# Performance work log

Measured on AMD Instinct MI355X. Metric: run time of the kernel, lower is better.

The kernel has to match this reference:

```python
import jax, jax.numpy as jnp
import numpy as np

H = 12            # heads
NB_FEATURES = 256 # Performer random features
EPS = 1e-4        # performer_pytorch softmax_kernel eps


def _gaussian_orthogonal_matrix(nb_rows, nb_cols, rng):
    # performer_pytorch gaussian_orthogonal_random_matrix, scaling=0
    nb_full = nb_rows // nb_cols
    blocks = []
    for _ in range(nb_full):
        q, _ = np.linalg.qr(rng.standard_normal((nb_cols, nb_cols)))
        blocks.append(q.T)
    rem = nb_rows - nb_full * nb_cols
    if rem > 0:
        q, _ = np.linalg.qr(rng.standard_normal((nb_cols, nb_cols)))
        blocks.append(q.T[:rem])
    M = np.concatenate(blocks, axis=0)
    multiplier = np.linalg.norm(rng.standard_normal((nb_rows, nb_cols)), axis=1)
    return (multiplier[:, None] * M).astype(np.float32)


def setup_inputs() -> dict:
    key = jax.random.key(0)
    ks = jax.random.split(key, 10)
    B, N, D = 8, 2048, 768
    s = D ** -0.5  # keep activations O(1) so exp() in FAVOR+ is stable
    inp = {
        "x": jax.random.normal(ks[0], (B, N, D), jnp.float32),
        "Wq": jax.random.normal(ks[1], (D, D), jnp.float32) * s,
        "bq": jnp.zeros((D,), jnp.float32),
        "Wk": jax.random.normal(ks[2], (D, D), jnp.float32) * s,
        "bk": jnp.zeros((D,), jnp.float32),
        "Wv": jax.random.normal(ks[3], (D, D), jnp.float32) * s,
        "bv": jnp.zeros((D,), jnp.float32),
        "Wo": jax.random.normal(ks[4], (D, D), jnp.float32) * s,
        "bo": jnp.zeros((D,), jnp.float32),
        "proj": jnp.asarray(_gaussian_orthogonal_matrix(NB_FEATURES, D // H, np.random.default_rng(0))),
    }
    return inp


def _softmax_kernel(x, proj, is_query):
    # x: [b,h,n,d], proj: [m,d] -> phi(x): [b,h,n,m]
    d = x.shape[-1]
    data_normalizer = d ** -0.25
    ratio = proj.shape[0] ** -0.5
    xp = jnp.einsum('bhnd,md->bhnm', x * data_normalizer, proj)
    diag = jnp.sum(x * x, axis=-1, keepdims=True) * 0.5 * (data_normalizer ** 2)
    if is_query:
        m = jax.lax.stop_gradient(jnp.max(xp, axis=-1, keepdims=True))
    else:
        m = jax.lax.stop_gradient(jnp.max(xp, axis=(-1, -2), keepdims=True))
    return ratio * (jnp.exp(xp - diag - m) + EPS)


def reference(x, Wq, bq, Wk, bk, Wv, bv, Wo, bo, proj):
    b, n, dim = x.shape
    d = dim // H
    # qkv projections, split into heads: [b,h,n,d]
    q = (x @ Wq.T + bq).reshape(b, n, H, d).transpose(0, 2, 1, 3)
    k = (x @ Wk.T + bk).reshape(b, n, H, d).transpose(0, 2, 1, 3)
    v = (x @ Wv.T + bv).reshape(b, n, H, d).transpose(0, 2, 1, 3)
    # FAVOR+ feature maps: [b,h,n,m]
    qp = _softmax_kernel(q, proj, True)
    kp = _softmax_kernel(k, proj, False)
    # non-causal linear attention
    k_sum = kp.sum(axis=2)                                  # [b,h,m]
    D_inv = 1.0 / jnp.einsum('bhnm,bhm->bhn', qp, k_sum)    # [b,h,n]
    ctx = jnp.einsum('bhnm,bhnd->bhmd', kp, v)              # [b,h,m,d]
    out = jnp.einsum('bhmd,bhnm,bhn->bhnd', ctx, qp, D_inv)
    out = out.transpose(0, 2, 1, 3).reshape(b, n, dim)
    return out @ Wo.T + bo
```

## Files before the change

### kernel.cpp

```cpp
#include <hip/hip_runtime.h>
#include <stdint.h>

typedef unsigned short u16;
typedef unsigned int u32;
typedef __attribute__((ext_vector_type(8))) short short8;
typedef __attribute__((ext_vector_type(4))) float floatx4;

#define HN 12
#define DH 64
#define DM 768
#define NS 2048
#define NB 8
#define MF 256
#define BN (NB*NS)
#define BH (NB*HN)

#define NRM 0.35355339059327373f
#define RATIO 0.0625f
#define EPSV 1e-4f

__device__ __forceinline__ float b2f(u32 u){ union{u32 i; float f;} x; x.i=u<<16; return x.f; }
__device__ __forceinline__ u32 f2b(float v){ union{float f; u32 u;} x; x.f=v; return (x.u + 0x7FFFu + ((x.u>>16)&1u))>>16; }
__device__ __forceinline__ u32 fkey(float v){ union{float f; u32 u;} x; x.f=v; return (x.u&0x80000000u)? ~x.u : (x.u|0x80000000u); }
__device__ __forceinline__ float funkey(u32 k){ union{u32 u; float f;} x; x.u=(k&0x80000000u)? (k^0x80000000u) : ~k; return x.f; }
__device__ __forceinline__ void bld8(uint4 r, float s, float* f){
  f[0]=b2f(r.x&0xffffu)*s; f[1]=b2f(r.x>>16)*s;
  f[2]=b2f(r.y&0xffffu)*s; f[3]=b2f(r.y>>16)*s;
  f[4]=b2f(r.z&0xffffu)*s; f[5]=b2f(r.z>>16)*s;
  f[6]=b2f(r.w&0xffffu)*s; f[7]=b2f(r.w>>16)*s;
}
__device__ __forceinline__ void load8(const void* base, size_t idx, int isf32, float s, float* f){
  if(isf32){
    const float* p=(const float*)base + idx;
    const float4 u=((const float4*)p)[0], v=((const float4*)p)[1];
    f[0]=u.x*s; f[1]=u.y*s; f[2]=u.z*s; f[3]=u.w*s;
    f[4]=v.x*s; f[5]=v.y*s; f[6]=v.z*s; f[7]=v.w*s;
  }else{
    uint4 r=*(const uint4*)((const u16*)base+idx);
    bld8(r,s,f);
  }
}
__device__ __forceinline__ float ld1(const void* base, int idx, int isf32){
  return isf32 ? ((const float*)base)[idx] : b2f((u32)((const u16*)base)[idx]);
}
__device__ __forceinline__ void gl16(const void* g, void* l){
  __builtin_amdgcn_global_load_lds(
    (const __attribute__((address_space(1))) u32*)g,
    (__attribute__((address_space(3))) u32*)l, 16, 0, 0);
}

__global__ __launch_bounds__(64) void k_detect(const u16* __restrict__ x, int* __restrict__ flag)
{
  __shared__ int w[64], z[64];
  const int t=threadIdx.x;
  int wild=0, zero=0;
  for(int i=t;i<256;i+=64){
    u32 u=(u32)x[2*i];
    u32 e=(u>>7)&0xFFu;
    if(e>=0x90u) wild++;
    if((u&0x7FFFu)==0u) zero++;
  }
  w[t]=wild; z[t]=zero; __syncthreads();
  if(t==0){
    int W=0,Z=0;
    for(int i=0;i<64;++i){W+=w[i];Z+=z[i];}
    flag[0]=(W>16||Z>200)?1:0;
  }
}

__global__ __launch_bounds__(256) void k_cvtw(const void* __restrict__ Wq,
    const void* __restrict__ Wk, const void* __restrict__ Wv, const void* __restrict__ Wo,
    u16* __restrict__ wb, u16* __restrict__ wob, const int* __restrict__ flagp)
{
  const int isf32=*flagp;
  const size_t WSZ=(size_t)DM*DM;
  size_t idx=((size_t)blockIdx.x*256+threadIdx.x)*8;
  const void* src; size_t off; u16* dst;
  if(idx<3*WSZ){ int w=(int)(idx/WSZ); src=(w==0)?Wq:((w==1)?Wk:Wv); off=idx-(size_t)w*WSZ; dst=wb+idx; }
  else { src=Wo; off=idx-3*WSZ; dst=wob+off; }
  if(isf32){
    const float* p=(const float*)src+off;
    float4 u=((const float4*)p)[0], v=((const float4*)p)[1];
    uint4 st;
    st.x=f2b(u.x)|(f2b(u.y)<<16); st.y=f2b(u.z)|(f2b(u.w)<<16);
    st.z=f2b(v.x)|(f2b(v.y)<<16); st.w=f2b(v.z)|(f2b(v.w)<<16);
    *(uint4*)dst=st;
  }else{
    *(uint4*)dst=*(const uint4*)((const u16*)src+off);
  }
}

__global__ __launch_bounds__(256) void k_cvtp(const void* __restrict__ proj,
    u16* __restrict__ pn, const int* __restrict__ flagp)
{
  const int isf32=*flagp;
  const size_t idx=((size_t)blockIdx.x*256+threadIdx.x)*8;
  float pf[8];
  load8(proj, idx, isf32, NRM, pf);
  uint4 st;
  st.x=f2b(pf[0])|(f2b(pf[1])<<16); st.y=f2b(pf[2])|(f2b(pf[3])<<16);
  st.z=f2b(pf[4])|(f2b(pf[5])<<16); st.w=f2b(pf[6])|(f2b(pf[7])<<16);
  *(uint4*)(pn+idx)=st;
}

__global__ __launch_bounds__(256) void k_cvtx(const void* __restrict__ x,
    u16* __restrict__ xb, const int* __restrict__ flagp)
{
  const int isf32=*flagp;
  const size_t idx=((size_t)blockIdx.x*256+threadIdx.x)*8;
  float f[8];
  load8(x, idx, isf32, 1.0f, f);
  uint4 st;
  st.x=f2b(f[0])|(f2b(f[1])<<16); st.y=f2b(f[2])|(f2b(f[3])<<16);
  st.z=f2b(f[4])|(f2b(f[5])<<16); st.w=f2b(f[6])|(f2b(f[7])<<16);
  *(uint4*)(xb+idx)=st;
}

__global__ __launch_bounds__(256) void k_diag(const u16* __restrict__ src, float* __restrict__ dk)
{
  const size_t row=(size_t)blockIdx.x*256+threadIdx.x;
  const u16* p=src+row*DH;
  float s=0.f;
#pragma unroll
  for(int c=0;c<DH;c+=8){
    uint4 r=*(const uint4*)(p+c);
    float f[8]; bld8(r,1.0f,f);
#pragma unroll
    for(int j=0;j<8;++j) s+=f[j]*f[j];
  }
  dk[row]=0.5f*NRM*NRM*s;
}

__device__ __forceinline__ void gemm_epilogue(const floatx4 acc[4][4], int mode, int oflag,
    int m0, int n0, int l, int wr4, int wc4,
    const void* bias0, const void* bias1, const void* bias2,
    u16* q, u16* k, u16* v, void* outv)
{
  const int rbase=(l>>4)*4, cl=l&15;
  if(mode==0){
    const int which=n0/DM;
    const void* bias=(which==0)?bias0:((which==1)?bias1:bias2);
    u16* outp=(which==0)?q:((which==1)?k:v);
    const int cb=n0-which*DM;
#pragma unroll
    for(int j=0;j<4;++j){
      const int col=cb+(wc4+j)*16+cl;
      const int h=col>>6, dd=col&63;
      const float bb=ld1(bias,col,oflag);
#pragma unroll
      for(int i=0;i<4;++i){
#pragma unroll
        for(int r=0;r<4;++r){
          const int grow=m0+(wr4+i)*16+rbase+r;
          const int b_=grow>>11, n=grow&2047;
          const u16 val=(u16)f2b(acc[i][j][r]+bb);
          if(which==2) outp[((size_t)(b_*HN+h)*DH+dd)*NS + n]=val;
          else         outp[((size_t)((b_*HN+h)*NS+n))*DH + dd]=val;
        }
      }
    }
  }else{
#pragma unroll
    for(int j=0;j<4;++j){
      const int col=n0+(wc4+j)*16+cl;
      const float bb=ld1(bias0,col,oflag);
#pragma unroll
      for(int i=0;i<4;++i){
#pragma unroll
        for(int r=0;r<4;++r){
          const int grow=m0+(wr4+i)*16+rbase+r;
          const float val=acc[i][j][r]+bb;
          if(oflag) ((float*)outv)[(size_t)grow*DM+col]=val;
          else      ((u16*)outv)[(size_t)grow*DM+col]=(u16)f2b(val);
        }
      }
    }
  }
}

__global__ __launch_bounds__(256) void k_gemm2(const u16* __restrict__ A16,
    const u16* __restrict__ B16,
    const void* __restrict__ bias0, const void* __restrict__ bias1, const void* __restrict__ bias2,
    u16* __restrict__ q, u16* __restrict__ k, u16* __restrict__ v,
    void* __restrict__ outv, const int* __restrict__ flagp, const int mode)
{
  __shared__ short At[16*512];
  __shared__ short Bt[16*512];
  const int oflag=*flagp;
  const int t=threadIdx.x, l=t&63, w=t>>6;
  const int m0=blockIdx.x*128, n0=blockIdx.y*128;
  const int wr4=(w>>1)*4, wc4=(w&1)*4;
  const int srow=l&15, skg=l>>4;
  floatx4 acc[4][4]={};
  for(int k0=0;k0<DM;k0+=64){
    __syncthreads();
#pragma unroll
    for(int s=0;s<4;++s){
      const int bi=w*4+s, rb=bi>>1, kh=bi&1;
      const int kc=k0+kh*32+skg*8;
      gl16(A16 + (size_t)(m0+rb*16+srow)*DM + kc, &At[bi*512]);
      gl16(B16 + (size_t)(n0+rb*16+srow)*DM + kc, &Bt[bi*512]);
    }
    __syncthreads();
#pragma unroll
    for(int kh=0;kh<2;++kh){
      short8 af[4], bf[4];
#pragma unroll
      for(int i=0;i<4;++i) af[i]=*(short8*)&At[((wr4+i)*2+kh)*512+l*8];
#pragma unroll
      for(int j=0;j<4;++j) bf[j]=*(short8*)&Bt[((wc4+j)*2+kh)*512+l*8];
#pragma unroll
      for(int i=0;i<4;++i)
#pragma unroll
        for(int j=0;j<4;++j)
          acc[i][j]=__builtin_amdgcn_mfma_f32_16x16x32_bf16(af[i],bf[j],acc[i][j],0,0,0);
    }
  }
  gemm_epilogue(acc,mode,oflag,m0,n0,l,wr4,wc4,bias0,bias1,bias2,q,k,v,outv);
}

__global__ __launch_bounds__(256) void k_gemm_f(const void* __restrict__ Araw,
    const u16* __restrict__ B16,
    const void* __restrict__ bias0, const void* __restrict__ bias1, const void* __restrict__ bias2,
    u16* __restrict__ q, u16* __restrict__ k, u16* __restrict__ v,
    void* __restrict__ outv, const int* __restrict__ flagp, const int mode)
{
  __shared__ short At[16*512];
  __shared__ short Bt[16*512];
  const int oflag=*flagp;
  const int isf32=(mode==0)?oflag:0;
  const int t=threadIdx.x, l=t&63, w=t>>6;
  const int m0=blockIdx.x*128, n0=blockIdx.y*128;
  const int wr4=(w>>1)*4, wc4=(w&1)*4;
  const int srow=l&15, skg=l>>4;
  floatx4 acc[4][4]={};
  for(int k0=0;k0<DM;k0+=64){
    __syncthreads();
#pragma unroll
    for(int s=0;s<4;++s){
      const int bi=w*4+s, rb=bi>>1, kh=bi&1;
      const int kc=k0+kh*32+skg*8;
      uint4 va;
      if(isf32){
        const float* ap=(const float*)Araw + (size_t)(m0+rb*16+srow)*DM + kc;
        float4 u=((const float4*)ap)[0], vv=((const float4*)ap)[1];
        va.x=f2b(u.x)|(f2b(u.y)<<16);  va.y=f2b(u.z)|(f2b(u.w)<<16);
        va.z=f2b(vv.x)|(f2b(vv.y)<<16); va.w=f2b(vv.z)|(f2b(vv.w)<<16);
      }else{
        va=*(const uint4*)((const u16*)Araw + (size_t)(m0+rb*16+srow)*DM + kc);
      }
      const uint4 vb=*(const uint4*)(B16 + (size_t)(n0+rb*16+srow)*DM + kc);
      *(uint4*)&At[bi*512+l*8]=va;
      *(uint4*)&Bt[bi*512+l*8]=vb;
    }
    __syncthreads();
#pragma unroll
    for(int kh=0;kh<2;++kh){
      short8 af[4], bf[4];
#pragma unroll
      for(int i=0;i<4;++i) af[i]=*(short8*)&At[((wr4+i)*2+kh)*512+l*8];
#pragma unroll
      for(int j=0;j<4;++j) bf[j]=*(short8*)&Bt[((wc4+j)*2+kh)*512+l*8];
#pragma unroll
      for(int i=0;i<4;++i)
#pragma unroll
        for(int j=0;j<4;++j)
          acc[i][j]=__builtin_amdgcn_mfma_f32_16x16x32_bf16(af[i],bf[j],acc[i][j],0,0,0);
    }
  }
  gemm_epilogue(acc,mode,oflag,m0,n0,l,wr4,wc4,bias0,bias1,bias2,q,k,v,outv);
}

#define SBOFF(slot,kh,mf) ((((slot)*32)+((kh)*16)+(mf))*512)
#define STA(kt,kh) do{ \
  const int o_=SBOFF((kt)&1,(kh),0); \
  const size_t g_=(size_t)(kt)*64+(size_t)(kh)*32; \
  gl16(Ar0+g_, &As[o_+w*512]); \
  gl16(Ar0+(size_t)128*768+g_, &As[o_+(8+w)*512]); \
}while(0)
#define STB(kt,kh) do{ \
  const int o_=SBOFF((kt)&1,(kh),0); \
  const size_t g_=(size_t)(kt)*64+(size_t)(kh)*32; \
  gl16(Br0+g_, &Bs[o_+w*512]); \
  gl16(Br0+(size_t)128*768+g_, &Bs[o_+(8+w)*512]); \
}while(0)
#define STAB(kt,kh) do{ STA(kt,kh); STB(kt,kh); }while(0)
#define LDA8(kt,kh) do{ const int o_=SBOFF((kt)&1,(kh),wr*8)+l*8; \
  _Pragma("unroll") for(int i_=0;i_<8;++i_) a[i_]=*(short8*)&As[o_+i_*512]; }while(0)
#define LDB4(kt,kh) do{ const int o_=SBOFF((kt)&1,(kh),wc*4)+l*8; \
  b[0]=*(short8*)&Bs[o_]; b[1]=*(short8*)&Bs[o_+512]; \
  b[2]=*(short8*)&Bs[o_+1024]; b[3]=*(short8*)&Bs[o_+1536]; }while(0)
#define MM(np) do{ _Pragma("unroll") for(int i_=0;i_<8;++i_){ \
  acc[i_][(np)*2+0]=__builtin_amdgcn_mfma_f32_16x16x32_bf16(a[i_],b[(np)*2+0],acc[i_][(np)*2+0],0,0,0); \
  acc[i_][(np)*2+1]=__builtin_amdgcn_mfma_f32_16x16x32_bf16(a[i_],b[(np)*2+1],acc[i_][(np)*2+1],0,0,0); } }while(0)
#define FEN asm volatile("" ::: "memory")
#define BARR do{ FEN; __builtin_amdgcn_s_barrier(); FEN; }while(0)
#define WV8 asm volatile("s_waitcnt vmcnt(8)" ::: "memory")
#define WV4 asm volatile("s_waitcnt vmcnt(4)" ::: "memory")
#define WV0 asm volatile("s_waitcnt vmcnt(0)" ::: "memory")
#define WL0 do{ asm volatile("s_waitcnt lgkmcnt(0)" ::: "memory"); __builtin_amdgcn_sched_barrier(0); }while(0)
#define PH4(kt,kh,SST,WST) do{ LDA8(kt,kh); LDB4(kt,kh); SST; WST; BARR; WL0; \
  __builtin_amdgcn_s_setprio(1); MM(0); MM(1); __builtin_amdgcn_s_setprio(0); BARR; }while(0)

__global__ __launch_bounds__(512,2) void k_gemm8(const u16* __restrict__ A16,
    const u16* __restrict__ B16,
    const void* __restrict__ bias0, const void* __restrict__ bias1, const void* __restrict__ bias2,
    u16* __restrict__ q, u16* __restrict__ k, u16* __restrict__ v,
    void* __restrict__ outv, const int* __restrict__ flagp, const int mode,
    float* __restrict__ dq_, float* __restrict__ dk_)
{
  __shared__ short As[2*2*16*512];
  __shared__ short Bs[2*2*16*512];
  const int oflag=*flagp;
  const int t=threadIdx.x, l=t&63, w=t>>6;
  const int wr=w>>2, wc=w&3;
  const int lrow=l&15, lk8=(l>>4)*8;
  int bid = blockIdx.y*gridDim.x + blockIdx.x;
  const int nwg = gridDim.x*gridDim.y;
  const int nN  = gridDim.y;
  bid = (bid&7)*(nwg>>3) + (bid>>3);
  const int mi = bid/nN;
  const int m0 = mi*256;
  const int n0 = (bid - mi*nN)*256;

  const u16* Ar0 = A16 + (size_t)(m0 + w*16 + lrow)*768 + lk8;
  const u16* Br0 = B16 + (size_t)(n0 + w*16 + lrow)*768 + lk8;
  floatx4 acc[8][4]={};
  short8 a[8], b[4];

  STA(0,0); STB(0,0); STA(0,1); STB(0,1); STA(1,0); STB(1,0);
  WV8; BARR;

  for(int i=0;i<5;++i){
    const int kt=2*i;
    PH4(kt,0,   STAB(kt+1,1), WV8);
    PH4(kt,1,   STAB(kt+2,0), WV8);
    PH4(kt+1,0, STAB(kt+2,1), WV8);
    PH4(kt+1,1, STAB(kt+3,0), WV8);
  }
  PH4(10,0, STAB(11,1), WV8);
  PH4(10,1, (void)0, WV4);
  PH4(11,0, (void)0, WV0);
  PH4(11,1, (void)0, (void)0);

  const int cl=l&15, q4=l>>4;
  if(mode==0){
    const int which=n0/DM;
    const int cb0=n0-which*DM;
    const void* bias=(which==0)?bias0:((which==1)?bias1:bias2);
    u16* outp=(which==0)?q:((which==1)?k:v);
    if(which==2){
#pragma unroll
      for(int j=0;j<4;++j){
        const int col=wc*64+j*16+cl;
        const float bb=ld1(bias,cb0+col,oflag);
        char* cbase=(char*)((col<128)? (void*)(As+col*256) : (void*)(Bs+(col-128)*256));
        const int X=(col&7)<<4;
#pragma unroll
        for(int i=0;i<8;++i){
          const int rowb=wr*128+i*16+q4*4;
          uint2 pk;
          pk.x=f2b(acc[i][j][0]+bb)|(f2b(acc[i][j][1]+bb)<<16);
          pk.y=f2b(acc[i][j][2]+bb)|(f2b(acc[i][j][3]+bb)<<16);
          *(uint2*)(cbase + ((rowb*2)^X)) = pk;
        }
      }
      __syncthreads();
      const int b_=m0>>11, nbase=m0&2047;
#pragma unroll
      for(int tt=0;tt<16;++tt){
        const int task=tt*8+w;
        const int colg=task>>2, qq=task&3;
        const int col=colg*8+(l>>3), sub=l&7;
        char* cbase=(char*)((col<128)? (void*)(As+col*256) : (void*)(Bs+(col-128)*256));
        const uint4 d4=*(const uint4*)(cbase + ((qq*128+sub*16)^((col&7)<<4)));
        const int gcol=cb0+col, h=gcol>>6, dd=gcol&63;
        const int n=nbase+qq*64+sub*8;
        *(uint4*)&outp[((size_t)(b_*HN+h)*DH+dd)*NS + n]=d4;
      }
    } else {
      float bb4[4];
#pragma unroll
      for(int j=0;j<4;++j) bb4[j]=ld1(bias, cb0+wc*64+j*16+cl, oflag);
      float* dptr=(which==0)? dq_ : dk_;
#pragma unroll
      for(int i=0;i<8;++i){
#pragma unroll
        for(int r=0;r<4;++r){
          const int row=wr*128+i*16+q4*4+r;
          char* rbase=(char*)((row<128)? (void*)(As+row*256) : (void*)(Bs+(row-128)*256));
          const int X=(row&3)<<4;
          float s=0.f;
#pragma unroll
          for(int j=0;j<4;++j){
            const int col=wc*64+j*16+cl;
            const u16 hv=(u16)f2b(acc[i][j][r]+bb4[j]);
            *(u16*)(rbase + ((col*2)^X)) = hv;
            const float fv=b2f(hv);
            s+=fv*fv;
          }
          s+=__shfl_xor(s,1,64); s+=__shfl_xor(s,2,64);
          s+=__shfl_xor(s,4,64); s+=__shfl_xor(s,8,64);
          if(cl==0){
            const int grow=m0+row, b_=grow>>11, n=grow&2047;
            dptr[(size_t)(b_*HN + (cb0>>6)+wc)*NS + n]=0.5f*NRM*NRM*s;
          }
        }
      }
      __syncthreads();
      const int hb=cb0>>6;
#pragma unroll
      for(int tt=0;tt<16;++tt){
        const int task=tt*8+w;
        const int rowg=task>>2, qq=task&3;
        const int row=rowg*8+(l>>3), sub=l&7;
        char* rbase=(char*)((row<128)? (void*)(As+row*256) : (void*)(Bs+(row-128)*256));
        const uint4 d4=*(const uint4*)(rbase + ((qq*128+sub*16)^((row&3)<<4)));
        const int grow=m0+row, b_=grow>>11, n=grow&2047;
        *(uint4*)&outp[((size_t)(b_*HN+hb+qq)*NS+n)*DH + sub*8]=d4;
      }
    }
  } else {
    if(oflag){
#pragma unroll
      for(int p=0;p<2;++p){
        if(wr==p){
#pragma unroll
          for(int j=0;j<4;++j){
            const int col=wc*64+j*16+cl;
            const float bb=ld1(bias0,n0+col,oflag);
#pragma unroll
            for(int i=0;i<8;++i){
#pragma unroll
              for(int r=0;r<4;++r){
                const int row=i*16+q4*4+r;
                char* rbase=(char*)((row<64)? (void*)(As+row*512) : (void*)(Bs+(row-64)*512));
                *(float*)(rbase + ((col*4)^((row&3)<<4))) = acc[i][j][r]+bb;
              }
            }
          }
        }
        __syncthreads();
#pragma unroll
        for(int tt=0;tt<16;++tt){
          const int task=tt*8+w;
          const int rowg=task>>3, qq=task&7;
          const int row=rowg*8+(l>>3), sub=l&7;
          char* rbase=(char*)((row<64)? (void*)(As+row*512) : (void*)(Bs+(row-64)*512));
          const uint4 d4=*(const uint4*)(rbase + ((qq*128+sub*16)^((row&3)<<4)));
          const size_t grow=(size_t)m0+p*128+row;
          *(uint4*)((char*)outv + (grow*DM+n0)*4 + qq*128 + sub*16)=d4;
        }
        __syncthreads();
      }
    } else {
#pragma unroll
      for(int j=0;j<4;++j){
        const int col=wc*64+j*16+cl;
        const float bb=ld1(bias0,n0+col,oflag);
#pragma unroll
        for(int i=0;i<8;++i){
#pragma unroll
          for(int r=0;r<4;++r){
            const int row=wr*128+i*16+q4*4+r;
            char* rbase=(char*)((row<128)? (void*)(As+row*256) : (void*)(Bs+(row-128)*256));
            *(u16*)(rbase + ((col*2)^((row&3)<<4))) = (u16)f2b(acc[i][j][r]+bb);
          }
        }
      }
      __syncthreads();
#pragma unroll
      for(int tt=0;tt<16;++tt){
        const int task=tt*8+w;
        const int rowg=task>>2, qq=task&3;
        const int row=rowg*8+(l>>3), sub=l&7;
        char* rbase=(char*)((row<128)? (void*)(As+row*256) : (void*)(Bs+(row-128)*256));
        const uint4 d4=*(const uint4*)(rbase + ((qq*128+sub*16)^((row&3)<<4)));
        const int grow=m0+row;
        *(uint4*)((u16*)outv + (size_t)grow*DM + n0 + qq*64 + sub*8)=d4;
      }
    }
  }
}

__global__ __launch_bounds__(256) void k_xpk2(const u16* __restrict__ kb,
    const u16* __restrict__ pn, u32* __restrict__ kmax)
{
  __shared__ short Bt[32*512];
  __shared__ short At[8*512];
  __shared__ float red[256];
  const int t=threadIdx.x, l=t&63, w=t>>6;
  const int bh=blockIdx.y, nb0=blockIdx.x*256;
  for(int s=t;s<2048;s+=256){
    const int ub=s>>6, l2=s&63, mt=ub>>1, kh=ub&1;
    const int row=mt*16+(l2&15), kc=kh*32+(l2>>4)*8;
    *(uint4*)&Bt[ub*512+l2*8]=*(const uint4*)(pn + (size_t)row*DH + kc);
  }
  float vmax=-3.4e38f;
  for(int c=0;c<4;++c){
    const int n0=nb0+c*64;
    __syncthreads();
    for(int s=t;s<512;s+=256){
      const int ua=s>>6, l2=s&63, rb=ua>>1, kh=ua&1;
      const int n=n0+rb*16+(l2&15), kc=kh*32+(l2>>4)*8;
      *(uint4*)&At[ua*512+l2*8]=*(const uint4*)(kb + ((size_t)bh*NS+n)*DH + kc);
    }
    __syncthreads();
    const short8 af0=*(short8*)&At[(w*2+0)*512+l*8];
    const short8 af1=*(short8*)&At[(w*2+1)*512+l*8];
#pragma unroll
    for(int mt=0;mt<16;++mt){
      floatx4 a={};
      a=__builtin_amdgcn_mfma_f32_16x16x32_bf16(af0,*(short8*)&Bt[(mt*2+0)*512+l*8],a,0,0,0);
      a=__builtin_amdgcn_mfma_f32_16x16x32_bf16(af1,*(short8*)&Bt[(mt*2+1)*512+l*8],a,0,0,0);
      vmax=fmaxf(vmax,fmaxf(fmaxf(a[0],a[1]),fmaxf(a[2],a[3])));
    }
  }
  red[t]=vmax; __syncthreads();
  for(int s=128;s>0;s>>=1){ if(t<s) red[t]=fmaxf(red[t],red[t+s]); __syncthreads(); }
  if(t==0) atomicMax(kmax+bh, fkey(red[0]));
}

__global__ __launch_bounds__(256) void k_ctx2(const u16* __restrict__ kb,
    const u16* __restrict__ vT, const u16* __restrict__ pn,
    const float* __restrict__ dkbuf, const u32* __restrict__ kmax,
    float* __restrict__ ctxT, float* __restrict__ ksum)
{
  __shared__ short Bt[32*512];
  __shared__ u16   Ks[256*72];
  __shared__ short AtV[8*512];
  __shared__ float dg[64];
  const int t=threadIdx.x, l=t&63, w=t>>6;
  const int split=blockIdx.x, bh=blockIdx.y;
  for(int s=t;s<2048;s+=256){
    const int ub=s>>6, l2=s&63, mt=ub>>1, kh=ub&1;
    const int row=mt*16+(l2&15), kc=kh*32+(l2>>4)*8;
    *(uint4*)&Bt[ub*512+l2*8]=*(const uint4*)(pn + (size_t)row*DH + kc);
  }
  const float kM=funkey(kmax[bh]);
  float ksr=0.f;
  floatx4 acc2[4][4]={};
  for(int c=0;c<8;++c){
    const int n0=split*512+c*64;
    __syncthreads();
    for(int s=t;s<512;s+=256){
      const int ua=s>>6, l2=s&63, rb=ua>>1, kh=ua&1;
      const int n=n0+rb*16+(l2&15), kc=kh*32+(l2>>4)*8;
      *(uint4*)&AtV[ua*512+l2*8]=*(const uint4*)(kb + ((size_t)bh*NS+n)*DH + kc);
    }
    if(t<64) dg[t]=dkbuf[(size_t)bh*NS+n0+t];
    __syncthreads();
    short8 af[4][2];
#pragma unroll
    for(int rb=0;rb<4;++rb){
      af[rb][0]=*(short8*)&AtV[(rb*2+0)*512+l*8];
      af[rb][1]=*(short8*)&AtV[(rb*2+1)*512+l*8];
    }
    float dgl[16];
#pragma unroll
    for(int rb=0;rb<4;++rb)
#pragma unroll
      for(int r=0;r<4;++r) dgl[rb*4+r]=dg[rb*16+(l>>4)*4+r];
#pragma unroll
    for(int ml=0;ml<4;++ml){
      const int mt=w*4+ml;
      const short8 bf0=*(short8*)&Bt[(mt*2+0)*512+l*8];
      const short8 bf1=*(short8*)&Bt[(mt*2+1)*512+l*8];
      const int m=mt*16+(l&15);
#pragma unroll
      for(int rb=0;rb<4;++rb){
        floatx4 a={};
        a=__builtin_amdgcn_mfma_f32_16x16x32_bf16(af[rb][0],bf0,a,0,0,0);
        a=__builtin_amdgcn_mfma_f32_16x16x32_bf16(af[rb][1],bf1,a,0,0,0);
        const int nb=rb*16+(l>>4)*4;
        const float v0=RATIO*(__expf(a[0]-dgl[rb*4+0]-kM)+EPSV);
        const float v1=RATIO*(__expf(a[1]-dgl[rb*4+1]-kM)+EPSV);
        const float v2=RATIO*(__expf(a[2]-dgl[rb*4+2]-kM)+EPSV);
        const float v3=RATIO*(__expf(a[3]-dgl[rb*4+3]-kM)+EPSV);
        *(u32*)&Ks[m*72+nb]  =f2b(v0)|(f2b(v1)<<16);
        *(u32*)&Ks[m*72+nb+2]=f2b(v2)|(f2b(v3)<<16);
      }
    }
    __syncthreads();
    for(int s=t;s<512;s+=256){
      const int uv=s>>6, l2=s&63, dt=uv>>1, kh=uv&1;
      const int d=dt*16+(l2&15), nn=n0+kh*32+(l2>>4)*8;
      *(uint4*)&AtV[uv*512+l2*8]=*(const uint4*)(vT + ((size_t)bh*DH+d)*NS + nn);
    }
    {
      float s8=0.f;
#pragma unroll
      for(int j=0;j<8;++j){
        const uint4 kk=*(const uint4*)&Ks[t*72+j*8];
        s8+=b2f(kk.x&0xffffu)+b2f(kk.x>>16)+b2f(kk.y&0xffffu)+b2f(kk.y>>16)
           +b2f(kk.z&0xffffu)+b2f(kk.z>>16)+b2f(kk.w&0xffffu)+b2f(kk.w>>16);
      }
      ksr+=s8;
    }
    __syncthreads();
#pragma unroll
    for(int i=0;i<4;++i){
      const int row=(w*4+i)*16+(l&15);
      const short8 a0=*(short8*)&Ks[row*72 + 0*32+(l>>4)*8];
      const short8 a1=*(short8*)&Ks[row*72 + 1*32+(l>>4)*8];
#pragma unroll
      for(int dt=0;dt<4;++dt){
        acc2[i][dt]=__builtin_amdgcn_mfma_f32_16x16x32_bf16(a0,*(short8*)&AtV[(dt*2+0)*512+l*8],acc2[i][dt],0,0,0);
        acc2[i][dt]=__builtin_amdgcn_mfma_f32_16x16x32_bf16(a1,*(short8*)&AtV[(dt*2+1)*512+l*8],acc2[i][dt],0,0,0);
      }
    }
  }
#pragma unroll
  for(int i=0;i<4;++i){
#pragma unroll
    for(int dt=0;dt<4;++dt){
#pragma unroll
      for(int r=0;r<4;++r){
        const int m=(w*4+i)*16+(l>>4)*4+r;
        const int d=dt*16+(l&15);
        atomicAdd(&ctxT[((size_t)bh*DH+d)*MF+m], acc2[i][dt][r]);
      }
    }
  }
  atomicAdd(ksum+bh*MF+t, ksr);
}

__global__ __launch_bounds__(256,2) void k_ctx3(const u16* __restrict__ kb,
    const u16* __restrict__ vT, const u16* __restrict__ pn,
    const float* __restrict__ dkbuf, const u32* __restrict__ kmax,
    float* __restrict__ ctxP, float* __restrict__ ksumP)
{
  __shared__ __align__(16) char SM[66048];
  short* Ks=(short*)SM;
  short* Kb=(short*)(SM+32768);
  short* Vb=(short*)(SM+49152);
  float* dgb=(float*)(SM+65536);
  const int t=threadIdx.x, l=t&63, w=t>>6;
  const int split=blockIdx.x, bh=blockIdx.y;
  const int n00=split*512;
  const int lrow=l&15, lk8=(l>>4)*8;
  const u16* kbase = kb + (size_t)bh*NS*DH;
  const u16* vbase = vT + (size_t)bh*DH*NS;
  short8 bf[4][2];
#pragma unroll
  for(int ml=0;ml<4;++ml)
#pragma unroll
    for(int kh=0;kh<2;++kh)
      bf[ml][kh]=*(const short8*)(pn + (size_t)((w*4+ml)*16+lrow)*DH + kh*32 + lk8);
  const float kM=funkey(kmax[bh]);
  {
#pragma unroll
    for(int p=0;p<2;++p){
      const int u=w+4*p, rb=u>>1, kh=u&1;
      gl16(kbase + (size_t)(n00+rb*16+lrow)*DH + kh*32+lk8, &Kb[u*512]);
    }
#pragma unroll
    for(int p=0;p<2;++p){
      const int u=w+4*p, dt=u>>1, kh=u&1;
      gl16(vbase + (size_t)(dt*16+lrow)*NS + n00+kh*32+lk8, &Vb[u*512]);
    }
    if(t<64) dgb[t]=dkbuf[(size_t)bh*NS+n00+t];
  }
  __syncthreads();
  float ksr=0.f;
  floatx4 acc2[4][4]={};
  for(int c=0;c<8;++c){
    const int cur=c&1, nxt=cur^1;
    if(c<7){
      const int n1=n00+(c+1)*64;
#pragma unroll
      for(int p=0;p<2;++p){
        const int u=w+4*p, rb=u>>1, kh=u&1;
        gl16(kbase + (size_t)(n1+rb*16+lrow)*DH + kh*32+lk8, &Kb[nxt*4096+u*512]);
      }
#pragma unroll
      for(int p=0;p<2;++p){
        const int u=w+4*p, dt=u>>1, kh=u&1;
        gl16(vbase + (size_t)(dt*16+lrow)*NS + n1+kh*32+lk8, &Vb[nxt*4096+u*512]);
      }
    }
    float dgnv=0.f;
    if(c<7 && t<64) dgnv=dkbuf[(size_t)bh*NS+n00+(c+1)*64+t];
    short8 af[4][2];
#pragma unroll
    for(int rb=0;rb<4;++rb){
      af[rb][0]=*(short8*)&Kb[cur*4096+(rb*2+0)*512+l*8];
      af[rb][1]=*(short8*)&Kb[cur*4096+(rb*2+1)*512+l*8];
    }
    float dgl[16];
#pragma unroll
    for(int rb=0;rb<4;++rb){
      const float4 dv=*(const float4*)&dgb[cur*64+rb*16+(l>>4)*4];
      dgl[rb*4+0]=dv.x; dgl[rb*4+1]=dv.y; dgl[rb*4+2]=dv.z; dgl[rb*4+3]=dv.w;
    }
#pragma unroll
    for(int ml=0;ml<4;++ml){
      const int m=(w*4+ml)*16+lrow;
      char* krow=(char*)Ks + m*128;
      const int xr=(m&7)<<4;
#pragma unroll
      for(int rb=0;rb<4;++rb){
        floatx4 a={};
        a=__builtin_amdgcn_mfma_f32_16x16x32_bf16(af[rb][0],bf[ml][0],a,0,0,0);
        a=__builtin_amdgcn_mfma_f32_16x16x32_bf16(af[rb][1],bf[ml][1],a,0,0,0);
        const float v0=RATIO*(__expf(a[0]-dgl[rb*4+0]-kM)+EPSV);
        const float v1=RATIO*(__expf(a[1]-dgl[rb*4+1]-kM)+EPSV);
        const float v2=RATIO*(__expf(a[2]-dgl[rb*4+2]-kM)+EPSV);
        const float v3=RATIO*(__expf(a[3]-dgl[rb*4+3]-kM)+EPSV);
        const int nb=rb*16+(l>>4)*4;
        const u32 bo=((u32)(nb*2)) ^ xr;
        *(u32*)(krow+bo)  =f2b(v0)|(f2b(v1)<<16);
        *(u32*)(krow+bo+4)=f2b(v2)|(f2b(v3)<<16);
      }
    }
    __syncthreads();
    {
      char* krow=(char*)Ks + t*128;
      const int xr=(t&7)<<4;
      float s8=0.f;
#pragma unroll
      for(int j=0;j<8;++j){
        const uint4 kk=*(const uint4*)(krow + ((j*16)^xr));
        s8+=b2f(kk.x&0xffffu)+b2f(kk.x>>16)+b2f(kk.y&0xffffu)+b2f(kk.y>>16)
           +b2f(kk.z&0xffffu)+b2f(kk.z>>16)+b2f(kk.w&0xffffu)+b2f(kk.w>>16);
      }
      ksr+=s8;
    }
#pragma unroll
    for(int i=0;i<4;++i){
      const int row=(w*4+i)*16+lrow;
      char* krow=(char*)Ks + row*128;
      const int xr=(row&7)<<4;
      const short8 a0=*(short8*)(krow + (((l>>4)*16)^xr));
      const short8 a1=*(short8*)(krow + ((64+(l>>4)*16)^xr));
#pragma unroll
      for(int dt=0;dt<4;++dt){
        acc2[i][dt]=__builtin_amdgcn_mfma_f32_16x16x32_bf16(a0,*(short8*)&Vb[cur*4096+(dt*2+0)*512+l*8],acc2[i][dt],0,0,0);
        acc2[i][dt]=__builtin_amdgcn_mfma_f32_16x16x32_bf16(a1,*(short8*)&Vb[cur*4096+(dt*2+1)*512+l*8],acc2[i][dt],0,0,0);
      }
    }
    if(c<7 && t<64) dgb[nxt*64+t]=dgnv;
    __syncthreads();
  }
  {
    float* OUT=(float*)SM;
#pragma unroll
    for(int i=0;i<4;++i){
      const int mb=(w*4+i)*16+(l>>4)*4;
#pragma unroll
      for(int dt=0;dt<4;++dt){
        const int d=dt*16+lrow;
        float4 o; o.x=acc2[i][dt][0]; o.y=acc2[i][dt][1]; o.z=acc2[i][dt][2]; o.w=acc2[i][dt][3];
        *(float4*)((char*)OUT + d*1024 + ((mb*4)^((d&15)<<4))) = o;
      }
    }
    __syncthreads();
    float* gout = ctxP + (size_t)(split*BH+bh)*64*256;
#pragma unroll
    for(int s=0;s<16;++s){
      const int d=s*4+w;
      const uint4 o4=*(const uint4*)((char*)OUT + d*1024 + ((l*16)^((d&15)<<4)));
      *(uint4*)(gout + (size_t)d*256 + l*4)=o4;
    }
    ksumP[(size_t)(split*BH+bh)*256 + t]=ksr;
  }
}

__global__ __launch_bounds__(256) void k_csplit(const float* __restrict__ ctxT,
    u16* __restrict__ chi, u16* __restrict__ clo, float* __restrict__ ecs)
{
  __shared__ float cred[256];
  const int bh=blockIdx.x, t=threadIdx.x;
  const int d=t>>2, part=t&3;
  const size_t base=((size_t)bh*DH+d)*MF + part*64;
  const float* src=ctxT + base;
  u16* ph=chi + base;
  u16* pl=clo + base;
  float cs=0.f;
  for(int m=0;m<64;m+=4){
    float4 v=*(const float4*)(src+m);
    float vv[4]={v.x,v.y,v.z,v.w};
    u32 h_[4], l_[4];
#pragma unroll
    for(int j=0;j<4;++j){
      cs+=vv[j];
      u32 hh=f2b(vv[j]);
      float rr=vv[j]-b2f(hh);
      h_[j]=hh; l_[j]=f2b(rr);
    }
    uint2 sh, sl;
    sh.x=h_[0]|(h_[1]<<16); sh.y=h_[2]|(h_[3]<<16);
    sl.x=l_[0]|(l_[1]<<16); sl.y=l_[2]|(l_[3]<<16);
    *(uint2*)(ph+m)=sh; *(uint2*)(pl+m)=sl;
  }
  cred[t]=cs; __syncthreads();
  if(part==0) ecs[bh*64+d]=EPSV*(cred[t]+cred[t+1]+cred[t+2]+cred[t+3]);
}

__global__ __launch_bounds__(256) void k_csplit3(const float* __restrict__ ctxP,
    const float* __restrict__ ksumP,
    u16* __restrict__ chi, u16* __restrict__ clo, float* __restrict__ ecs,
    float* __restrict__ ksum)
{
  __shared__ float wred[16][4];
  const int bh=blockIdx.y, dq=blockIdx.x;
  const int t=threadIdx.x, l=t&63, w=t>>6;
  if(dq==0){
    float kv=0.f;
#pragma unroll
    for(int s=0;s<4;++s) kv+=ksumP[(size_t)(s*BH+bh)*256+t];
    ksum[bh*MF+t]=kv;
  }
#pragma unroll
  for(int d16=0;d16<16;++d16){
    const int d=dq*16+d16;
    float v=0.f;
#pragma unroll
    for(int s=0;s<4;++s) v+=ctxP[((size_t)(s*BH+bh)*64+d)*256+t];
    const u32 hh=f2b(v);
    const float rr=v-b2f(hh);
    const size_t ob=((size_t)bh*DH+d)*MF+t;
    chi[ob]=(u16)hh; clo[ob]=(u16)f2b(rr);
    float s_=v;
    s_+=__shfl_xor(s_,1,64); s_+=__shfl_xor(s_,2,64); s_+=__shfl_xor(s_,4,64);
    s_+=__shfl_xor(s_,8,64); s_+=__shfl_xor(s_,16,64); s_+=__shfl_xor(s_,32,64);
    if(l==0) wred[d16][w]=s_;
  }
  __syncthreads();
  if(t<16) ecs[bh*64+dq*16+t]=EPSV*(wred[t][0]+wred[t][1]+wred[t][2]+wred[t][3]);
}

__global__ __launch_bounds__(256) void k_attn2(const u16* __restrict__ qb,
    const u16* __restrict__ pn, const float* __restrict__ dqbuf,
    const float* __restrict__ ksum, const u16* __restrict__ chi, const u16* __restrict__ clo,
    const float* __restrict__ ecs, u16* __restrict__ attn)
{
  __shared__ short At[8*512];
  __shared__ u16 Qf[32*512];
  __shared__ float ksums[256];
  __shared__ float dq_s[64];
  __shared__ float mxs[4][64];
  __shared__ float s1s[4][64];
  __shared__ float a_s[64], dinv_s[64], ec_s[64];
  __shared__ float red4[4];
  __shared__ float epkss;
  const int t=threadIdx.x, l=t&63, w=t>>6;
  const int bh=blockIdx.y, nb0=blockIdx.x*256;
  const int b_=bh/HN, h=bh%HN;
  {
    float kv=ksum[bh*MF+t];
    ksums[t]=kv;
    if(t<64) ec_s[t]=ecs[bh*64+t];
    float s=kv;
#pragma unroll
    for(int o=1;o<64;o<<=1) s+=__shfl_xor(s,o,64);
    if(l==0) red4[w]=s;
  }
  __syncthreads();
  if(t==0) epkss=EPSV*(red4[0]+red4[1]+red4[2]+red4[3]);
  short8 bhf[8], blf[8];
  {
    const int d=w*16+(l&15);
    const size_t base=((size_t)bh*DH+d)*MF;
#pragma unroll
    for(int kc=0;kc<8;++kc){
      const size_t off=base + kc*32+(l>>4)*8;
      bhf[kc]=*(const short8*)(chi+off);
      blf[kc]=*(const short8*)(clo+off);
    }
  }
  for(int c=0;c<4;++c){
    const int n0c=nb0+c*64;
    __syncthreads();
    for(int s=t;s<512;s+=256){
      const int ua=s>>6, l2=s&63, nt=ua>>1, kh=ua&1;
      const int n=n0c+nt*16+(l2&15), kc=kh*32+(l2>>4)*8;
      *(uint4*)&At[ua*512+l2*8]=*(const uint4*)(qb + ((size_t)bh*NS+n)*DH + kc);
    }
    if(t<64) dq_s[t]=dqbuf[(size_t)bh*NS+n0c+t];
    __syncthreads();
    float mxl[4]={-3.4e38f,-3.4e38f,-3.4e38f,-3.4e38f};
    float s1l[4]={0.f,0.f,0.f,0.f};
#pragma unroll
    for(int mt=0;mt<4;++mt){
      const int gm=w*4+mt;
      const u16* pr=pn + ((gm*16+(l&15))<<6) + (l>>4)*8;
      const short8 a0=*(const short8*)(pr);
      const short8 a1=*(const short8*)(pr+32);
      float k4[4];
#pragma unroll
      for(int r=0;r<4;++r) k4[r]=ksums[gm*16+(l>>4)*4+r];
      const int mbase=(gm&1)*16+(l>>4)*4;
      const int lane2=((mbase>>3)*16+(l&15))*8 + (mbase&7);
#pragma unroll
      for(int nt=0;nt<4;++nt){
        floatx4 xp={};
        xp=__builtin_amdgcn_mfma_f32_16x16x32_bf16(a0,*(short8*)&At[(nt*2+0)*512+l*8],xp,0,0,0);
        xp=__builtin_amdgcn_mfma_f32_16x16x32_bf16(a1,*(short8*)&At[(nt*2+1)*512+l*8],xp,0,0,0);
        const float dq=dq_s[nt*16+(l&15)];
        float ev[4];
#pragma unroll
        for(int r=0;r<4;++r){
          const float xv=xp[r];
          mxl[nt]=fmaxf(mxl[nt],xv);
          ev[r]=__expf(xv-dq);
          s1l[nt]+=ev[r]*k4[r];
        }
        u16* qp_=&Qf[(nt*8+(gm>>1))*512 + lane2];
        *(u32*)qp_    =f2b(ev[0])|(f2b(ev[1])<<16);
        *(u32*)(qp_+2)=f2b(ev[2])|(f2b(ev[3])<<16);
      }
    }
#pragma unroll
    for(int nt=0;nt<4;++nt){
      float m_=mxl[nt], s_=s1l[nt];
      m_=fmaxf(m_,__shfl_xor(m_,16,64)); s_+=__shfl_xor(s_,16,64);
      m_=fmaxf(m_,__shfl_xor(m_,32,64)); s_+=__shfl_xor(s_,32,64);
      if(l<16){ mxs[w][nt*16+l]=m_; s1s[w][nt*16+l]=s_; }
    }
    __syncthreads();
    if(t<64){
      float m_=fmaxf(fmaxf(mxs[0][t],mxs[1][t]),fmaxf(mxs[2][t],mxs[3][t]));
      float s_=s1s[0][t]+s1s[1][t]+s1s[2][t]+s1s[3][t];
      float a=__expf(-m_);
      a_s[t]=a;
      dinv_s[t]=1.0f/(a*s_+epkss);
    }
    __syncthreads();
    const int d=w*16+(l&15);
    const float ec=ec_s[d];
#pragma unroll
    for(int nt=0;nt<4;++nt){
      floatx4 y={};
#pragma unroll
      for(int kc=0;kc<8;++kc){
        const short8 e=*(short8*)&Qf[(nt*8+kc)*512+l*8];
        y=__builtin_amdgcn_mfma_f32_16x16x32_bf16(e,bhf[kc],y,0,0,0);
        y=__builtin_amdgcn_mfma_f32_16x16x32_bf16(e,blf[kc],y,0,0,0);
      }
#pragma unroll
      for(int r=0;r<4;++r){
        const int nl=nt*16+(l>>4)*4+r;
        const float val=(a_s[nl]*y[r]+ec)*dinv_s[nl];
        attn[((size_t)(b_*NS+n0c+nl))*DM + h*DH + d]=(u16)f2b(val);
      }
    }
  }
}

extern "C" void kernel_launch(void* const* d_in, const int* in_sizes, int n_in,
                              void* d_out, int out_size, void* d_ws, size_t ws_size,
                              hipStream_t stream)
{
  (void)in_sizes; (void)n_in; (void)out_size;
  const void* x =d_in[0];
  const void* Wq=d_in[1]; const void* bq=d_in[2];
  const void* Wk=d_in[3]; const void* bk=d_in[4];
  const void* Wv=d_in[5]; const void* bv=d_in[6];
  const void* Wo=d_in[7]; const void* bo=d_in[8];
  const void* proj=d_in[9];

  char* ws=(char*)d_ws;
  const size_t SZ=(size_t)BN*DM*2;
  const size_t AUXSZ=19030528;
  const bool big = ws_size >= 4*SZ + AUXSZ;
  u16*   qb  =(u16*)(ws);
  u16*   kb  =(u16*)(ws+SZ);
  u16*   vb  =(u16*)(ws+2*SZ);
  u16*   xb  =(u16*)(ws+3*SZ);
  char*  aux = big ? (ws+4*SZ) : (ws+3*SZ);
  u16*   wb   =(u16*)(aux);
  u16*   wob  =(u16*)(aux+3538944);
  float* ctxT =(float*)(aux+4718592);
  float* ksum =(float*)(aux+11010048);
  u32*   kmax =(u32*)(aux+11108352);
  int*   flag =(int*)(aux+11108736);
  float* dk   =(float*)(aux+11108864);
  float* dqq  =(float*)(aux+11895296);
  u16*   pn   =(u16*)(aux+12681728);
  u16*   chi  =(u16*)(aux+12714496);
  u16*   clo  =(u16*)(aux+15860224);
  float* ecs  =(float*)(aux+19005952);
  u16*   attnb = big ? xb : kb;

  k_detect<<<1,64,0,stream>>>((const u16*)x, flag);
  if(big) hipMemsetAsync(kmax, 0, 384, stream);
  else    hipMemsetAsync(ctxT, 0, 6291456+98304+384, stream);
  k_cvtw <<<1152, 256, 0, stream>>>(Wq,Wk,Wv,Wo,wb,wob,flag);
  k_cvtp <<<8, 256, 0, stream>>>(proj, pn, flag);
  if(big){
    k_cvtx <<<(BN*DM)/2048, 256, 0, stream>>>(x, xb, flag);
    k_gemm8<<<dim3(BN/256,2304/256), 512, 0, stream>>>(xb, wb, bq,bk,bv, qb,kb,vb, nullptr, flag, 0, dqq, dk);
  }else{
    k_gemm_f<<<dim3(BN/128,2304/128), 256, 0, stream>>>(x, wb, bq,bk,bv, qb,kb,vb, nullptr, flag, 0);
    k_diag <<<(BH*NS)/256, 256, 0, stream>>>(kb, dk);
    k_diag <<<(BH*NS)/256, 256, 0, stream>>>(qb, dqq);
  }
  k_xpk2 <<<dim3(NS/256,BH), 256, 0, stream>>>(kb, pn, kmax);
  if(big){
    float* ctxP =(float*)xb;
    float* ksumP=ctxT;
    k_ctx3 <<<dim3(4,BH), 256, 0, stream>>>(kb, vb, pn, dk, kmax, ctxP, ksumP);
    k_csplit3<<<dim3(4,BH), 256, 0, stream>>>(ctxP, ksumP, chi, clo, ecs, ksum);
  }else{
    k_ctx2 <<<dim3(4,BH), 256, 0, stream>>>(kb, vb, pn, dk, kmax, ctxT, ksum);
    k_csplit<<<BH, 256, 0, stream>>>(ctxT, chi, clo, ecs);
  }
  k_attn2<<<dim3(NS/256,BH), 256, 0, stream>>>(qb, pn, dqq, ksum, chi, clo, ecs, attnb);
  if(big){
    k_gemm8<<<dim3(BN/256,DM/256), 512, 0, stream>>>(attnb, wob, bo,bo,bo, nullptr,nullptr,nullptr, d_out, flag, 1, nullptr, nullptr);
  }else{
    k_gemm2<<<dim3(BN/128,DM/128), 256, 0, stream>>>(attnb, wob, bo,bo,bo, nullptr,nullptr,nullptr, d_out, flag, 1);
  }
}
```

Before: 412.9 us.

## Replace 256x256 GEMM with 256x128 tile, triple-buffered K=32 pipeline

The bf16 GEMM used for the QKV and output projections now uses 256x128 output tiles instead of 256x256. Each of the eight waves owns a 64x64 sub-tile, and the K loop advances in steps of 32 through a three-slot shared-memory ring instead of a double buffer of K=64 halves. Occupancy hints go from two to four blocks per CU, and the grids double to 64x18 and 64x6 workgroups. The epilogues are rewritten for the smaller tile with a single LDS staging buffer and an 8-row XOR swizzle. The aim is more parallelism and latency hiding from smaller accumulators, at the cost of lower arithmetic intensity per tile and more barriers per unit of K.

```diff
diff --git a/kernel.cpp b/kernel.cpp
--- a/kernel.cpp
+++ b/kernel.cpp
@@ -271,49 +271,40 @@
   gemm_epilogue(acc,mode,oflag,m0,n0,l,wr4,wc4,bias0,bias1,bias2,q,k,v,outv);
 }
 
-#define SBOFF(slot,kh,mf) ((((slot)*32)+((kh)*16)+(mf))*512)
-#define STA(kt,kh) do{ \
-  const int o_=SBOFF((kt)&1,(kh),0); \
-  const size_t g_=(size_t)(kt)*64+(size_t)(kh)*32; \
-  gl16(Ar0+g_, &As[o_+w*512]); \
-  gl16(Ar0+(size_t)128*768+g_, &As[o_+(8+w)*512]); \
+#define G9OFF(s,u) (((s)*24+(u))*512)
+#define G9STA(kt,s) do{ \
+  const size_t g_=(size_t)(kt)*32; \
+  gl16(Ar0+g_, &LD[G9OFF(s,w)]); \
+  gl16(Ar0+(size_t)128*768+g_, &LD[G9OFF(s,8+w)]); \
+  gl16(Br0+g_, &LD[G9OFF(s,16+w)]); \
 }while(0)
-#define STB(kt,kh) do{ \
-  const int o_=SBOFF((kt)&1,(kh),0); \
-  const size_t g_=(size_t)(kt)*64+(size_t)(kh)*32; \
-  gl16(Br0+g_, &Bs[o_+w*512]); \
-  gl16(Br0+(size_t)128*768+g_, &Bs[o_+(8+w)*512]); \
+#define G9LD(s) do{ \
+  _Pragma("unroll") for(int i_=0;i_<4;++i_) a[i_]=*(short8*)&LD[G9OFF(s,wr4+i_)+l*8]; \
+  _Pragma("unroll") for(int j_=0;j_<4;++j_) b[j_]=*(short8*)&LD[G9OFF(s,16+wc4+j_)+l*8]; \
 }while(0)
-#define STAB(kt,kh) do{ STA(kt,kh); STB(kt,kh); }while(0)
-#define LDA8(kt,kh) do{ const int o_=SBOFF((kt)&1,(kh),wr*8)+l*8; \
-  _Pragma("unroll") for(int i_=0;i_<8;++i_) a[i_]=*(short8*)&As[o_+i_*512]; }while(0)
-#define LDB4(kt,kh) do{ const int o_=SBOFF((kt)&1,(kh),wc*4)+l*8; \
-  b[0]=*(short8*)&Bs[o_]; b[1]=*(short8*)&Bs[o_+512]; \
-  b[2]=*(short8*)&Bs[o_+1024]; b[3]=*(short8*)&Bs[o_+1536]; }while(0)
-#define MM(np) do{ _Pragma("unroll") for(int i_=0;i_<8;++i_){ \
-  acc[i_][(np)*2+0]=__builtin_amdgcn_mfma_f32_16x16x32_bf16(a[i_],b[(np)*2+0],acc[i_][(np)*2+0],0,0,0); \
-  acc[i_][(np)*2+1]=__builtin_amdgcn_mfma_f32_16x16x32_bf16(a[i_],b[(np)*2+1],acc[i_][(np)*2+1],0,0,0); } }while(0)
+#define G9MM do{ _Pragma("unroll") for(int i_=0;i_<4;++i_){ \
+  _Pragma("unroll") for(int j_=0;j_<4;++j_) \
+    acc[i_][j_]=__builtin_amdgcn_mfma_f32_16x16x32_bf16(a[i_],b[j_],acc[i_][j_],0,0,0); } }while(0)
 #define FEN asm volatile("" ::: "memory")
 #define BARR do{ FEN; __builtin_amdgcn_s_barrier(); FEN; }while(0)
-#define WV8 asm volatile("s_waitcnt vmcnt(8)" ::: "memory")
-#define WV4 asm volatile("s_waitcnt vmcnt(4)" ::: "memory")
+#define WV3 asm volatile("s_waitcnt vmcnt(3)" ::: "memory")
 #define WV0 asm volatile("s_waitcnt vmcnt(0)" ::: "memory")
 #define WL0 do{ asm volatile("s_waitcnt lgkmcnt(0)" ::: "memory"); __builtin_amdgcn_sched_barrier(0); }while(0)
-#define PH4(kt,kh,SST,WST) do{ LDA8(kt,kh); LDB4(kt,kh); SST; WST; BARR; WL0; \
-  __builtin_amdgcn_s_setprio(1); MM(0); MM(1); __builtin_amdgcn_s_setprio(0); BARR; }while(0)
-
-__global__ __launch_bounds__(512,2) void k_gemm8(const u16* __restrict__ A16,
+#define G9PH(kt,s,SST,WST) do{ G9LD(s); SST; WST; BARR; WL0; \
+  __builtin_amdgcn_s_setprio(1); G9MM; __builtin_amdgcn_s_setprio(0); BARR; }while(0)
+
+__global__ __launch_bounds__(512,4) void k_gemm9(const u16* __restrict__ A16,
     const u16* __restrict__ B16,
     const void* __restrict__ bias0, const void* __restrict__ bias1, const void* __restrict__ bias2,
     u16* __restrict__ q, u16* __restrict__ k, u16* __restrict__ v,
     void* __restrict__ outv, const int* __restrict__ flagp, const int mode,
     float* __restrict__ dq_, float* __restrict__ dk_)
 {
-  __shared__ short As[2*2*16*512];
-  __shared__ short Bs[2*2*16*512];
+  __shared__ short LD[3*24*512];
   const int oflag=*flagp;
   const int t=threadIdx.x, l=t&63, w=t>>6;
-  const int wr=w>>2, wc=w&3;
+  const int wr=w>>1, wc=w&1;
+  const int wr4=wr*4, wc4=wc*4;
   const int lrow=l&15, lk8=(l>>4)*8;
   int bid = blockIdx.y*gridDim.x + blockIdx.x;
   const int nwg = gridDim.x*gridDim.y;
@@ -321,81 +312,77 @@
   bid = (bid&7)*(nwg>>3) + (bid>>3);
   const int mi = bid/nN;
   const int m0 = mi*256;
-  const int n0 = (bid - mi*nN)*256;
+  const int n0 = (bid - mi*nN)*128;
 
   const u16* Ar0 = A16 + (size_t)(m0 + w*16 + lrow)*768 + lk8;
   const u16* Br0 = B16 + (size_t)(n0 + w*16 + lrow)*768 + lk8;
-  floatx4 acc[8][4]={};
-  short8 a[8], b[4];
-
-  STA(0,0); STB(0,0); STA(0,1); STB(0,1); STA(1,0); STB(1,0);
-  WV8; BARR;
-
-  for(int i=0;i<5;++i){
-    const int kt=2*i;
-    PH4(kt,0,   STAB(kt+1,1), WV8);
-    PH4(kt,1,   STAB(kt+2,0), WV8);
-    PH4(kt+1,0, STAB(kt+2,1), WV8);
-    PH4(kt+1,1, STAB(kt+3,0), WV8);
-  }
-  PH4(10,0, STAB(11,1), WV8);
-  PH4(10,1, (void)0, WV4);
-  PH4(11,0, (void)0, WV0);
-  PH4(11,1, (void)0, (void)0);
-
+  floatx4 acc[4][4]={};
+  short8 a[4], b[4];
+
+  G9STA(0,0); G9STA(1,1);
+  WV3; BARR;
+
+  for(int it=0; it<7; ++it){
+    const int kt=3*it;
+    G9PH(kt+0,0, G9STA(kt+2,2), WV3);
+    G9PH(kt+1,1, G9STA(kt+3,0), WV3);
+    G9PH(kt+2,2, G9STA(kt+4,1), WV3);
+  }
+  G9PH(21,0, G9STA(23,2), WV3);
+  G9PH(22,1, (void)0, WV0);
+  G9PH(23,2, (void)0, (void)0);
+
+  char* LB=(char*)LD;
   const int cl=l&15, q4=l>>4;
+  const int wrm=wr*64, wcn=wc*64;
   if(mode==0){
     const int which=n0/DM;
     const int cb0=n0-which*DM;
+    const int hb=cb0>>6;
     const void* bias=(which==0)?bias0:((which==1)?bias1:bias2);
     u16* outp=(which==0)?q:((which==1)?k:v);
     if(which==2){
 #pragma unroll
       for(int j=0;j<4;++j){
-        const int col=wc*64+j*16+cl;
+        const int col=wcn+j*16+cl;
         const float bb=ld1(bias,cb0+col,oflag);
-        char* cbase=(char*)((col<128)? (void*)(As+col*256) : (void*)(Bs+(col-128)*256));
         const int X=(col&7)<<4;
 #pragma unroll
-        for(int i=0;i<8;++i){
-          const int rowb=wr*128+i*16+q4*4;
+        for(int i=0;i<4;++i){
+          const int rowb=wrm+i*16+q4*4;
           uint2 pk;
           pk.x=f2b(acc[i][j][0]+bb)|(f2b(acc[i][j][1]+bb)<<16);
           pk.y=f2b(acc[i][j][2]+bb)|(f2b(acc[i][j][3]+bb)<<16);
-          *(uint2*)(cbase + ((rowb*2)^X)) = pk;
+          *(uint2*)(LB + col*512 + ((rowb*2)^X)) = pk;
         }
       }
       __syncthreads();
       const int b_=m0>>11, nbase=m0&2047;
 #pragma unroll
-      for(int tt=0;tt<16;++tt){
-        const int task=tt*8+w;
-        const int colg=task>>2, qq=task&3;
-        const int col=colg*8+(l>>3), sub=l&7;
-        char* cbase=(char*)((col<128)? (void*)(As+col*256) : (void*)(Bs+(col-128)*256));
-        const uint4 d4=*(const uint4*)(cbase + ((qq*128+sub*16)^((col&7)<<4)));
-        const int gcol=cb0+col, h=gcol>>6, dd=gcol&63;
-        const int n=nbase+qq*64+sub*8;
-        *(uint4*)&outp[((size_t)(b_*HN+h)*DH+dd)*NS + n]=d4;
+      for(int s8=0;s8<8;++s8){
+        const int c=s8*512+t;
+        const int col=c>>5, off=(c&31)*16;
+        const uint4 d4=*(const uint4*)(LB + col*512 + (off^((col&7)<<4)));
+        const int h=hb+(col>>6), dd=col&63;
+        *(uint4*)&outp[((size_t)(b_*HN+h)*DH+dd)*NS + nbase + (off>>1)]=d4;
       }
     } else {
       float bb4[4];
 #pragma unroll
-      for(int j=0;j<4;++j) bb4[j]=ld1(bias, cb0+wc*64+j*16+cl, oflag);
+      for(int j=0;j<4;++j) bb4[j]=ld1(bias, cb0+wcn+j*16+cl, oflag);
       float* dptr=(which==0)? dq_ : dk_;
 #pragma unroll
-      for(int i=0;i<8;++i){
+      for(int i=0;i<4;++i){
 #pragma unroll
         for(int r=0;r<4;++r){
-          const int row=wr*128+i*16+q4*4+r;
-          char* rbase=(char*)((row<128)? (void*)(As+row*256) : (void*)(Bs+(row-128)*256));
-          const int X=(row&3)<<4;
+          const int row=wrm+i*16+q4*4+r;
+          const int X=(row&7)<<4;
           float s=0.f;
 #pragma unroll
           for(int j=0;j<4;++j){
-            const int col=wc*64+j*16+cl;
+            const int col=wcn+j*16+cl;
             const u16 hv=(u16)f2b(acc[i][j][r]+bb4[j]);
-            *(u16*)(rbase + ((col*2)^X)) = hv;
+            *(u16*)(LB + row*256 + ((col*2)^X)) = hv;
             const float fv=b2f(hv);
             s+=fv*fv;
           }
@@ -403,81 +390,72 @@
           s+=__shfl_xor(s,4,64); s+=__shfl_xor(s,8,64);
           if(cl==0){
             const int grow=m0+row, b_=grow>>11, n=grow&2047;
-            dptr[(size_t)(b_*HN + (cb0>>6)+wc)*NS + n]=0.5f*NRM*NRM*s;
+            dptr[(size_t)(b_*HN + hb + wc)*NS + n]=0.5f*NRM*NRM*s;
           }
         }
       }
       __syncthreads();
-      const int hb=cb0>>6;
-#pragma unroll
-      for(int tt=0;tt<16;++tt){
-        const int task=tt*8+w;
-        const int rowg=task>>2, qq=task&3;
-        const int row=rowg*8+(l>>3), sub=l&7;
-        char* rbase=(char*)((row<128)? (void*)(As+row*256) : (void*)(Bs+(row-128)*256));
-        const uint4 d4=*(const uint4*)(rbase + ((qq*128+sub*16)^((row&3)<<4)));
+#pragma unroll
+      for(int s8=0;s8<8;++s8){
+        const int c=s8*512+t;
+        const int row=c>>4, off=(c&15)*16;
+        const uint4 d4=*(const uint4*)(LB + row*256 + (off^((row&7)<<4)));
         const int grow=m0+row, b_=grow>>11, n=grow&2047;
-        *(uint4*)&outp[((size_t)(b_*HN+hb+qq)*NS+n)*DH + sub*8]=d4;
+        *(uint4*)&outp[((size_t)((b_*HN+hb+(off>>7))*NS+n))*DH + ((off>>1)&63)]=d4;
       }
     }
   } else {
     if(oflag){
 #pragma unroll
       for(int p=0;p<2;++p){
-        if(wr==p){
+        if((wr>>1)==p){
+          const int rl0=(wr&1)*64;
 #pragma unroll
           for(int j=0;j<4;++j){
-            const int col=wc*64+j*16+cl;
+            const int col=wcn+j*16+cl;
             const float bb=ld1(bias0,n0+col,oflag);
 #pragma unroll
-            for(int i=0;i<8;++i){
+            for(int i=0;i<4;++i){
 #pragma unroll
               for(int r=0;r<4;++r){
-                const int row=i*16+q4*4+r;
-                char* rbase=(char*)((row<64)? (void*)(As+row*512) : (void*)(Bs+(row-64)*512));
-                *(float*)(rbase + ((col*4)^((row&3)<<4))) = acc[i][j][r]+bb;
+                const int rl=rl0+i*16+q4*4+r;
+                *(float*)(LB + rl*512 + ((col*4)^((rl&7)<<4))) = acc[i][j][r]+bb;
               }
             }
           }
         }
         __syncthreads();
 #pragma unroll
-        for(int tt=0;tt<16;++tt){
-          const int task=tt*8+w;
-          const int rowg=task>>3, qq=task&7;
-          const int row=rowg*8+(l>>3), sub=l&7;
-          char* rbase=(char*)((row<64)? (void*)(As+row*512) : (void*)(Bs+(row-64)*512));
-          const uint4 d4=*(const uint4*)(rbase + ((qq*128+sub*16)^((row&3)<<4)));
-          const size_t grow=(size_t)m0+p*128+row;
-          *(uint4*)((char*)outv + (grow*DM+n0)*4 + qq*128 + sub*16)=d4;
+        for(int s8=0;s8<8;++s8){
+          const int c=s8*512+t;
+          const int rl=c>>5, off=(c&31)*16;
+          const uint4 d4=*(const uint4*)(LB + rl*512 + (off^((rl&7)<<4)));
+          const size_t grow=(size_t)m0+p*128+rl;
+          *(uint4*)((char*)outv + (grow*DM+n0)*4 + off)=d4;
         }
         __syncthreads();
       }
     } else {
 #pragma unroll
       for(int j=0;j<4;++j){
-        const int col=wc*64+j*16+cl;
+        const int col=wcn+j*16+cl;
         const float bb=ld1(bias0,n0+col,oflag);
 #pragma unroll
-        for(int i=0;i<8;++i){
+        for(int i=0;i<4;++i){
 #pragma unroll
           for(int r=0;r<4;++r){
-            const int row=wr*128+i*16+q4*4+r;
-            char* rbase=(char*)((row<128)? (void*)(As+row*256) : (void*)(Bs+(row-128)*256));
-            *(u16*)(rbase + ((col*2)^((row&3)<<4))) = (u16)f2b(acc[i][j][r]+bb);
+            const int row=wrm+i*16+q4*4+r;
+            *(u16*)(LB + row*256 + ((col*2)^((row&7)<<4))) = (u16)f2b(acc[i][j][r]+bb);
           }
         }
       }
       __syncthreads();
 #pragma unroll
-      for(int tt=0;tt<16;++tt){
-        const int task=tt*8+w;
-        const int rowg=task>>2, qq=task&3;
-        const int row=rowg*8+(l>>3), sub=l&7;
-        char* rbase=(char*)((row<128)? (void*)(As+row*256) : (void*)(Bs+(row-128)*256));
-        const uint4 d4=*(const uint4*)(rbase + ((qq*128+sub*16)^((row&3)<<4)));
-        const int grow=m0+row;
-        *(uint4*)((u16*)outv + (size_t)grow*DM + n0 + qq*64 + sub*8)=d4;
+      for(int s8=0;s8<8;++s8){
+        const int c=s8*512+t;
+        const int row=c>>4, off=(c&15)*16;
+        const uint4 d4=*(const uint4*)(LB + row*256 + (off^((row&7)<<4)));
+        *(uint4*)((u16*)outv + (size_t)(m0+row)*DM + n0 + (off>>1))=d4;
       }
     }
   }
@@ -990,7 +968,7 @@
   k_cvtp <<<8, 256, 0, stream>>>(proj, pn, flag);
   if(big){
     k_cvtx <<<(BN*DM)/2048, 256, 0, stream>>>(x, xb, flag);
-    k_gemm8<<<dim3(BN/256,2304/256), 512, 0, stream>>>(xb, wb, bq,bk,bv, qb,kb,vb, nullptr, flag, 0, dqq, dk);
+    k_gemm9<<<dim3(64,18), 512, 0, stream>>>(xb, wb, bq,bk,bv, qb,kb,vb, nullptr, flag, 0, dqq, dk);
   }else{
     k_gemm_f<<<dim3(BN/128,2304/128), 256, 0, stream>>>(x, wb, bq,bk,bv, qb,kb,vb, nullptr, flag, 0);
     k_diag <<<(BH*NS)/256, 256, 0, stream>>>(kb, dk);
@@ -1008,7 +986,7 @@
   }
   k_attn2<<<dim3(NS/256,BH), 256, 0, stream>>>(qb, pn, dqq, ksum, chi, clo, ecs, attnb);
   if(big){
-    k_gemm8<<<dim3(BN/256,DM/256), 512, 0, stream>>>(attnb, wob, bo,bo,bo, nullptr,nullptr,nullptr, d_out, flag, 1, nullptr, nullptr);
+    k_gemm9<<<dim3(64,6), 512, 0, stream>>>(attnb, wob, bo,bo,bo, nullptr,nullptr,nullptr, d_out, flag, 1, nullptr, nullptr);
   }else{
     k_gemm2<<<dim3(BN/128,DM/128), 256, 0, stream>>>(attnb, wob, bo,bo,bo, nullptr,nullptr,nullptr, d_out, flag, 1);
   }
```

Measured after the change: 397.3 us, median of 2. 1.04x faster.
